# Kernel tuning notes

Hardware: AMD Instinct MI355X
Metric: run time of the kernel (lower is better)

Reference implementation:

```python
import jax, jax.numpy as jnp
import numpy as np

N = 20000      # nodes
E = 320000     # edges
S = 256        # scalar (0e) channels of irreps_feature
F = 960        # full irreps_feature dim (256x0e+128x1e+64x2e)
NB = 32        # number_of_basis
CUT = 5.0      # max_radius


def setup_inputs() -> dict:
    key = jax.random.key(0)
    ks = jax.random.split(key, 24)
    def w(k, shape):
        return jax.random.normal(k, shape, jnp.float32) / np.sqrt(shape[0])
    return {
        "node_feature": jax.random.normal(ks[0], (N, F), jnp.float32),
        "pos": jax.random.normal(ks[1], (N, 3), jnp.float32),
        "edge_index": jax.random.randint(ks[2], (2, E), 0, N),
        "W_ai1": w(ks[3], (S, S)), "b_ai1": jnp.zeros((S,), jnp.float32),
        "W_ai2": w(ks[4], (S, 1)), "b_ai2": jnp.zeros((1,), jnp.float32),
        "W_ci1": w(ks[5], (S, S)), "b_ci1": jnp.zeros((S,), jnp.float32),
        "W_ci2": w(ks[6], (S, 1)), "b_ci2": jnp.zeros((1,), jnp.float32),
        "W_sc": w(ks[7], (S, S)), "b_sc": jnp.zeros((S,), jnp.float32),
        "W_ed": w(ks[8], (NB, S)), "b_ed": jnp.zeros((S,), jnp.float32),
        "W_b1": w(ks[9], (3 * S, S)), "b_b1": jnp.zeros((S,), jnp.float32),
        "W_b2": w(ks[10], (S, 1)), "b_b2": jnp.zeros((1,), jnp.float32),
    }


def _rbf(d):
    # ExpNormalSmearing (torchmd-net), cutoff_lower=0, cutoff_upper=CUT, non-trainable
    start = np.exp(-CUT)
    means = jnp.linspace(start, 1.0, NB, dtype=jnp.float32)
    beta = jnp.float32(((2.0 / NB) * (1.0 - start)) ** -2)
    cosine_cut = 0.5 * (jnp.cos(np.pi * d / CUT) + 1.0) * (d < CUT)
    return cosine_cut[:, None] * jnp.exp(-beta * (jnp.exp(-d)[:, None] - means) ** 2)


def reference(node_feature, pos, edge_index,
              W_ai1, b_ai1, W_ai2, b_ai2,
              W_ci1, b_ci1, W_ci2, b_ci2,
              W_sc, b_sc, W_ed, b_ed,
              W_b1, b_b1, W_b2, b_b2):
    # LinearRS(irreps_feature -> 0e) only touches the 0e block (first S channels)
    scal = node_feature[:, :S]
    silu = jax.nn.silu

    log_ai = silu(scal @ W_ai1 + b_ai1) @ W_ai2 + b_ai2          # [N,1]
    ai = jnp.exp(log_ai)
    log_ci = silu(scal @ W_ci1 + b_ci1) @ W_ci2 + b_ci2          # [N,1]
    ci = jnp.exp(log_ci)

    src, dst = edge_index[0], edge_index[1]
    rel = pos[dst] - pos[src]                                     # [E,3]
    norm = jnp.linalg.norm(rel, axis=1, keepdims=True)            # [E,1]
    rhat = rel / (norm + 1e-8)
    emb = _rbf(norm[:, 0])                                        # [E,NB]

    node_sc = scal @ W_sc + b_sc                                  # project once, gather [N,S]
    src_f = node_sc[src]
    dst_f = node_sc[dst]
    edge_f = emb @ W_ed + b_ed
    edge_feature = jnp.concatenate([src_f, dst_f, edge_f], axis=-1)  # [E,3S]
    bij = silu(edge_feature @ W_b1 + b_b1) @ W_b2 + b_b2          # [E,1]

    # edge softmax over incoming edges of dst, with extra ci mass
    bmax = jax.ops.segment_max(bij, dst, num_segments=N)
    bmax = jnp.where(jnp.isneginf(bmax), 0.0, bmax)
    bij_exp = jnp.exp(bij - bmax[dst])
    bsum = jax.ops.segment_sum(bij_exp, dst, num_segments=N) + ci  # [N,1]
    gamma = bij_exp / (bsum[dst] + 1e-7)                           # [E,1]

    bij_prime = gamma * ai[dst]                                    # [E,1]
    outer = rhat[:, :, None] * rhat[:, None, :]                    # [E,3,3]
    contrib = jax.ops.segment_sum(bij_prime[:, :, None] * outer, dst, num_segments=N)  # [N,3,3]

    eye3 = jnp.eye(3, dtype=pos.dtype)
    sigma = ai[:, :, None] * eye3 - contrib + 1e-6 * eye3          # [N,3,3]
    sum_gamma = jax.ops.segment_sum(gamma, dst, num_segments=N)    # [N,1]
    return sigma, ai, sum_gamma
```

## Files before the change

### kernel.cpp

```cpp
#include <hip/hip_runtime.h>
#include <math.h>

#define N_NODES 20000
#define E_EDGES 320000
#define F_DIM   960
#define S_DIM   256
#define QTAB    2048
#define ASTRIDE 264
#define CAP     64
#define CPAD    66

typedef __attribute__((ext_vector_type(8))) short short8;
typedef __attribute__((ext_vector_type(4))) float f32x4;

__device__ __forceinline__ float siluf(float x) {
    return x / (1.0f + __expf(-x));
}

__device__ __forceinline__ unsigned short bf16rn(float x) {
    unsigned u = __float_as_uint(x);
    return (unsigned short)((u + 0x7FFFu + ((u >> 16) & 1u)) >> 16);
}

__device__ __forceinline__ void bf16x8_to_f32(short8 v8, float* o) {
    union { short8 s; uint4 u; } cv; cv.s = v8;
    o[0] = __uint_as_float(cv.u.x << 16);
    o[1] = __uint_as_float(cv.u.x & 0xffff0000u);
    o[2] = __uint_as_float(cv.u.y << 16);
    o[3] = __uint_as_float(cv.u.y & 0xffff0000u);
    o[4] = __uint_as_float(cv.u.z << 16);
    o[5] = __uint_as_float(cv.u.z & 0xffff0000u);
    o[6] = __uint_as_float(cv.u.w << 16);
    o[7] = __uint_as_float(cv.u.w & 0xffff0000u);
}

__global__ void prep_kernel(const float* __restrict__ W_sc, const float* __restrict__ W_ed,
                            const float* __restrict__ W_b1, const float* __restrict__ b_sc,
                            const float* __restrict__ b_ed, const float* __restrict__ b_b1,
                            const float* __restrict__ W_ai1, const float* __restrict__ W_ci1,
                            float* __restrict__ Bcat, float* __restrict__ We, float* __restrict__ c0,
                            int* __restrict__ cnt)
{
    int idx = blockIdx.x * 256 + threadIdx.x;
    if (idx < N_NODES) cnt[idx] = 0;
    if (idx < 256 * 1024) {
        int k = idx >> 10, j = idx & 1023;
        float s = 0.0f;
        if (j < 256) {
            for (int m = 0; m < 256; ++m) s += W_sc[k * 256 + m] * W_b1[m * 256 + j];
        } else if (j < 512) {
            int jj = j - 256;
            for (int m = 0; m < 256; ++m) s += W_sc[k * 256 + m] * W_b1[(256 + m) * 256 + jj];
        } else if (j < 768) {
            s = W_ai1[k * 256 + (j - 512)];
        } else {
            s = W_ci1[k * 256 + (j - 768)];
        }
        Bcat[idx] = s;
    } else if (idx < 256 * 1024 + 32 * 256) {
        int t = idx - 256 * 1024;
        int p = t >> 8, j = t & 255;
        float s = 0.0f;
        for (int m = 0; m < 256; ++m) s += W_ed[p * 256 + m] * W_b1[(512 + m) * 256 + j];
        We[t] = s;
    } else if (idx < 256 * 1024 + 32 * 256 + 256) {
        int j = idx - 256 * 1024 - 32 * 256;
        float s = b_b1[j];
        for (int m = 0; m < 256; ++m) {
            s += b_sc[m] * (W_b1[m * 256 + j] + W_b1[(256 + m) * 256 + j]);
            s += b_ed[m] * W_b1[(512 + m) * 256 + j];
        }
        c0[j] = s;
    }
}

__global__ void aux_kernel(const int* __restrict__ ei, int* __restrict__ cnt, int* __restrict__ rank,
                           const float* __restrict__ Bcat, unsigned short* __restrict__ Bpack,
                           const float* __restrict__ We, unsigned short* __restrict__ Tab,
                           const float* __restrict__ nf, unsigned short* __restrict__ scalp)
{
    int b = blockIdx.x;
    if (b < 1250) {
        int i = b * 256 + threadIdx.x;
        rank[i] = atomicAdd(&cnt[ei[E_EDGES + i]], 1);
    } else if (b < 1378) {
        int idx = (b - 1250) * 256 + threadIdx.x;
        int kq = idx & 3, j = (idx >> 2) & 1023, t = idx >> 12;
        #pragma unroll
        for (int jj = 0; jj < 8; ++jj)
            Bpack[idx * 8 + jj] = bf16rn(Bcat[(t * 32 + kq * 8 + jj) * 1024 + j]);
    } else if (b < 3426) {
        int idx = (b - 1378) * 256 + threadIdx.x;
        int q = idx >> 8, j = idx & 255;
        float nrm = 5.0f * (float)q / (float)(QTAB - 1);
        const float start = 0.006737946999085467f;
        const float mustep = (1.0f - start) / 31.0f;
        const float bx = (2.0f / 32.0f) * (1.0f - start);
        const float beta = 1.0f / (bx * bx);
        const float PI_F = 3.14159265358979323846f;
        float cc = (nrm < 5.0f) ? 0.5f * (cosf(PI_F * nrm * 0.2f) + 1.0f) : 0.0f;
        float t = expf(-nrm);
        float s = 0.0f;
        for (int k = 0; k < 32; ++k) {
            float dm = t - (start + (float)k * mustep);
            s += expf(-beta * dm * dm) * We[k * 256 + j];
        }
        Tab[idx] = bf16rn(cc * s);
    } else {
        int idx = (b - 3426) * 256 + threadIdx.x;
        int base = idx * 4;
        int n = base >> 8, k = base & 255;
        float4 a4 = *(const float4*)&nf[(size_t)n * F_DIM + k];
        ushort4 b4;
        b4.x = bf16rn(a4.x); b4.y = bf16rn(a4.y);
        b4.z = bf16rn(a4.z); b4.w = bf16rn(a4.w);
        *(ushort4*)&scalp[n * 256 + k] = b4;
    }
}

__global__ __launch_bounds__(1024) void scan_kernel(const int* __restrict__ cnt,
                                                    int* __restrict__ start)
{
    __shared__ int ps[1024];
    const int t = threadIdx.x;
    const int base = t * 20;
    int loc[20];
    int s = 0;
    #pragma unroll
    for (int i = 0; i < 20; ++i) {
        int n = (base + i < N_NODES) ? cnt[base + i] : 0;
        loc[i] = s; s += n;
    }
    ps[t] = s;
    __syncthreads();
    for (int off = 1; off < 1024; off <<= 1) {
        int v = (t >= off) ? ps[t - off] : 0;
        __syncthreads();
        ps[t] += v;
        __syncthreads();
    }
    int offset = ps[t] - s;
    #pragma unroll
    for (int i = 0; i < 20; ++i)
        if (base + i < N_NODES) start[base + i] = offset + loc[i];
}

__global__ void scatter_kernel(const int* __restrict__ ei, const int* __restrict__ start,
                               const int* __restrict__ rank, int* __restrict__ srcS)
{
    int i = blockIdx.x * 256 + threadIdx.x;
    if (i < E_EDGES) srcS[start[ei[E_EDGES + i]] + rank[i]] = ei[i];
}

__global__ __launch_bounds__(256) void node_mfma_kernel(
    const unsigned short* __restrict__ scalp, const unsigned short* __restrict__ Bpack,
    const float* __restrict__ c0,
    const float* __restrict__ b_ai1, const float* __restrict__ W_ai2, const float* __restrict__ b_ai2,
    const float* __restrict__ b_ci1, const float* __restrict__ W_ci2, const float* __restrict__ b_ci2,
    unsigned short* __restrict__ u, unsigned short* __restrict__ v,
    float* __restrict__ bsumseed, float* __restrict__ out_ai)
{
    __shared__ unsigned short A[32 * ASTRIDE];
    __shared__ float red[32 * 4];

    const int tid = threadIdx.x;
    const int w = tid >> 6, lane = tid & 63;
    const int bg = blockIdx.x & 3;
    const int m0 = (blockIdx.x >> 2) * 32;
    const int col16 = lane & 15, quad = lane >> 4;

    #pragma unroll
    for (int it = 0; it < 4; ++it) {
        int idx = (it * 256 + tid) * 8;
        int r = idx >> 8, c = idx & 255;
        *(uint4*)&A[r * ASTRIDE + c] = *(const uint4*)&scalp[(m0 + r) * 256 + c];
    }
    __syncthreads();

    f32x4 acc[2][4];
    #pragma unroll
    for (int mt = 0; mt < 2; ++mt)
        #pragma unroll
        for (int nt = 0; nt < 4; ++nt)
            acc[mt][nt] = (f32x4){0.0f, 0.0f, 0.0f, 0.0f};

    const int colbase = bg * 256 + w * 64;

    for (int t = 0; t < 8; ++t) {
        short8 af[2];
        #pragma unroll
        for (int mt = 0; mt < 2; ++mt)
            af[mt] = *(const short8*)&A[(mt * 16 + col16) * ASTRIDE + t * 32 + quad * 8];
        short8 bf[4];
        #pragma unroll
        for (int nt = 0; nt < 4; ++nt)
            bf[nt] = *(const short8*)&Bpack[(((t * 1024 + colbase + nt * 16 + col16) * 4) + quad) * 8];
        #pragma unroll
        for (int mt = 0; mt < 2; ++mt)
            #pragma unroll
            for (int nt = 0; nt < 4; ++nt)
                acc[mt][nt] = __builtin_amdgcn_mfma_f32_16x16x32_bf16(af[mt], bf[nt], acc[mt][nt], 0, 0, 0);
    }

    if (bg == 0) {
        #pragma unroll
        for (int nt = 0; nt < 4; ++nt) {
            int jl = w * 64 + nt * 16 + col16;
            float c0v = c0[jl];
            #pragma unroll
            for (int mt = 0; mt < 2; ++mt)
                #pragma unroll
                for (int reg = 0; reg < 4; ++reg)
                    u[(m0 + mt * 16 + quad * 4 + reg) * 256 + jl] = bf16rn(acc[mt][nt][reg] + c0v);
        }
    } else if (bg == 1) {
        #pragma unroll
        for (int nt = 0; nt < 4; ++nt) {
            int jl = w * 64 + nt * 16 + col16;
            #pragma unroll
            for (int mt = 0; mt < 2; ++mt)
                #pragma unroll
                for (int reg = 0; reg < 4; ++reg)
                    v[(m0 + mt * 16 + quad * 4 + reg) * 256 + jl] = bf16rn(acc[mt][nt][reg]);
        }
    } else {
        const float* b1 = (bg == 2) ? b_ai1 : b_ci1;
        const float* w2 = (bg == 2) ? W_ai2 : W_ci2;
        float s[2][4] = {{0, 0, 0, 0}, {0, 0, 0, 0}};
        #pragma unroll
        for (int nt = 0; nt < 4; ++nt) {
            int jl = w * 64 + nt * 16 + col16;
            float bb = b1[jl], ww = w2[jl];
            #pragma unroll
            for (int mt = 0; mt < 2; ++mt)
                #pragma unroll
                for (int reg = 0; reg < 4; ++reg)
                    s[mt][reg] += siluf(acc[mt][nt][reg] + bb) * ww;
        }
        #pragma unroll
        for (int off = 1; off < 16; off <<= 1) {
            #pragma unroll
            for (int mt = 0; mt < 2; ++mt)
                #pragma unroll
                for (int reg = 0; reg < 4; ++reg)
                    s[mt][reg] += __shfl_xor(s[mt][reg], off);
        }
        if (col16 == 0) {
            #pragma unroll
            for (int mt = 0; mt < 2; ++mt)
                #pragma unroll
                for (int reg = 0; reg < 4; ++reg)
                    red[(mt * 16 + quad * 4 + reg) * 4 + w] = s[mt][reg];
        }
        __syncthreads();
        if (tid < 32) {
            float sum = red[tid * 4] + red[tid * 4 + 1] + red[tid * 4 + 2] + red[tid * 4 + 3];
            if (bg == 2) out_ai[m0 + tid] = expf(sum + b_ai2[0]);
            else         bsumseed[m0 + tid] = expf(sum + b_ci2[0]) + 1e-7f;
        }
    }
}

__global__ __launch_bounds__(256) void edge_node_kernel(
    const int* __restrict__ start, const int* __restrict__ cnt, const int* __restrict__ srcS,
    const float* __restrict__ pos,
    const unsigned short* __restrict__ u, const unsigned short* __restrict__ v,
    const unsigned short* __restrict__ Tab, const float* __restrict__ W_b2, const float* __restrict__ b_b2,
    const float* __restrict__ bsumseed, const float* __restrict__ out_ai,
    float* __restrict__ out_sigma, float* __restrict__ out_sg)
{
    __shared__ float sb[16][CPAD];
    __shared__ float srx[16][CPAD];
    __shared__ float sry[16][CPAD];
    __shared__ float srz[16][CPAD];

    const int grp = threadIdx.x >> 4;
    const int l   = threadIdx.x & 15;
    const int g   = blockIdx.x * 16 + grp;
    const int st  = start[g];
    const int deg = min(cnt[g], CAP);

    float vch[16];
    bf16x8_to_f32(*(const short8*)&v[(size_t)g * 256 + l * 16], vch);
    bf16x8_to_f32(*(const short8*)&v[(size_t)g * 256 + l * 16 + 8], vch + 8);
    float w2c[16];
    #pragma unroll
    for (int c = 0; c < 16; c += 4)
        *(float4*)&w2c[c] = *(const float4*)&W_b2[l * 16 + c];
    const float bb2 = b_b2[0];
    const float gx = pos[3 * g + 0], gy = pos[3 * g + 1], gz = pos[3 * g + 2];
    const float xscale = (float)(QTAB - 1) * 0.2f;

    int s_cur = (deg > 0) ? srcS[st] : 0;
    float pxc = pos[3 * s_cur + 0], pyc = pos[3 * s_cur + 1], pzc = pos[3 * s_cur + 2];
    short8 u0c = *(const short8*)&u[(size_t)s_cur * 256 + l * 16];
    short8 u1c = *(const short8*)&u[(size_t)s_cur * 256 + l * 16 + 8];

    for (int i = 0; i < deg; ++i) {
        int s_nxt = (i + 1 < deg) ? srcS[st + i + 1] : s_cur;
        float pxn = pos[3 * s_nxt + 0], pyn = pos[3 * s_nxt + 1], pzn = pos[3 * s_nxt + 2];
        short8 u0n = *(const short8*)&u[(size_t)s_nxt * 256 + l * 16];
        short8 u1n = *(const short8*)&u[(size_t)s_nxt * 256 + l * 16 + 8];

        float px = gx - pxc, py = gy - pyc, pz = gz - pzc;
        float nrm = sqrtf(px * px + py * py + pz * pz);
        float inv = 1.0f / (nrm + 1e-8f);
        float rx = px * inv, ry = py * inv, rz = pz * inv;

        float x = nrm * xscale;
        int qi = (int)x;
        float f = x - (float)qi;
        if (qi >= QTAB - 1) { qi = QTAB - 2; f = 1.0f; }

        float acc = 0.0f;
        #pragma unroll
        for (int half = 0; half < 2; ++half) {
            float uf[8], t0f[8], t1f[8];
            bf16x8_to_f32(half ? u1c : u0c, uf);
            bf16x8_to_f32(*(const short8*)&Tab[(size_t)qi * 256 + l * 16 + half * 8], t0f);
            bf16x8_to_f32(*(const short8*)&Tab[(size_t)(qi + 1) * 256 + l * 16 + half * 8], t1f);
            #pragma unroll
            for (int c = 0; c < 8; ++c) {
                float h = uf[c] + vch[half * 8 + c] + t0f[c] + f * (t1f[c] - t0f[c]);
                float sig = __builtin_amdgcn_rcpf(1.0f + __expf(-h));
                acc += w2c[half * 8 + c] * h * sig;
            }
        }
        #pragma unroll
        for (int off = 1; off < 16; off <<= 1) acc += __shfl_xor(acc, off);

        if (l == 0) {
            sb[grp][i] = acc + bb2;
            srx[grp][i] = rx; sry[grp][i] = ry; srz[grp][i] = rz;
        }
        s_cur = s_nxt; pxc = pxn; pyc = pyn; pzc = pzn; u0c = u0n; u1c = u1n;
    }

    float m = -1e30f;
    for (int i = l; i < deg; i += 16) m = fmaxf(m, sb[grp][i]);
    #pragma unroll
    for (int off = 1; off < 16; off <<= 1) m = fmaxf(m, __shfl_xor(m, off));

    float ssum = 0.0f;
    for (int i = l; i < deg; i += 16) ssum += __expf(sb[grp][i] - m);
    #pragma unroll
    for (int off = 1; off < 16; off <<= 1) ssum += __shfl_xor(ssum, off);

    float invt = 1.0f / (ssum + bsumseed[g]);

    float a0 = 0, a1 = 0, a2 = 0, a3 = 0, a4 = 0, a5 = 0, a6 = 0;
    for (int i = l; i < deg; i += 16) {
        float gm = __expf(sb[grp][i] - m) * invt;
        float rx = srx[grp][i], ry = sry[grp][i], rz = srz[grp][i];
        a0 += gm * rx * rx; a1 += gm * ry * ry; a2 += gm * rz * rz;
        a3 += gm * rx * ry; a4 += gm * rx * rz; a5 += gm * ry * rz;
        a6 += gm;
    }
    #pragma unroll
    for (int off = 1; off < 16; off <<= 1) {
        a0 += __shfl_xor(a0, off); a1 += __shfl_xor(a1, off);
        a2 += __shfl_xor(a2, off); a3 += __shfl_xor(a3, off);
        a4 += __shfl_xor(a4, off); a5 += __shfl_xor(a5, off);
        a6 += __shfl_xor(a6, off);
    }

    if (l == 0) {
        float ai = out_ai[g];
        float* sg = &out_sigma[g * 9];
        float d0 = ai + 1e-6f;
        sg[0] = d0 - ai * a0;
        sg[1] = -ai * a3;
        sg[2] = -ai * a4;
        sg[3] = -ai * a3;
        sg[4] = d0 - ai * a1;
        sg[5] = -ai * a5;
        sg[6] = -ai * a4;
        sg[7] = -ai * a5;
        sg[8] = d0 - ai * a2;
        out_sg[g] = a6;
    }
}

extern "C" void kernel_launch(void* const* d_in, const int* in_sizes, int n_in,
                              void* d_out, int out_size, void* d_ws, size_t ws_size,
                              hipStream_t stream)
{
    const float* nf    = (const float*)d_in[0];
    const float* pos   = (const float*)d_in[1];
    const int*   ei    = (const int*)  d_in[2];
    const float* W_ai1 = (const float*)d_in[3];
    const float* b_ai1 = (const float*)d_in[4];
    const float* W_ai2 = (const float*)d_in[5];
    const float* b_ai2 = (const float*)d_in[6];
    const float* W_ci1 = (const float*)d_in[7];
    const float* b_ci1 = (const float*)d_in[8];
    const float* W_ci2 = (const float*)d_in[9];
    const float* b_ci2 = (const float*)d_in[10];
    const float* W_sc  = (const float*)d_in[11];
    const float* b_sc  = (const float*)d_in[12];
    const float* W_ed  = (const float*)d_in[13];
    const float* b_ed  = (const float*)d_in[14];
    const float* W_b1  = (const float*)d_in[15];
    const float* b_b1  = (const float*)d_in[16];
    const float* W_b2  = (const float*)d_in[17];
    const float* b_b2  = (const float*)d_in[18];

    char* pb = (char*)d_ws;
    auto alloc = [&](size_t bytes) -> void* {
        void* r = (void*)pb;
        pb += (bytes + 255) & ~(size_t)255;
        return r;
    };
    float*          Bcat    = (float*)         alloc(262144 * 4);
    float*          We      = (float*)         alloc(8192 * 4);
    float*          c0      = (float*)         alloc(256 * 4);
    unsigned short* Tab     = (unsigned short*)alloc((size_t)QTAB * 256 * 2);
    unsigned short* Bpack   = (unsigned short*)alloc((size_t)256 * 1024 * 2);
    unsigned short* scalp   = (unsigned short*)alloc((size_t)N_NODES * 256 * 2);
    unsigned short* u       = (unsigned short*)alloc((size_t)N_NODES * 256 * 2);
    unsigned short* v       = (unsigned short*)alloc((size_t)N_NODES * 256 * 2);
    float*          bsumseed= (float*)         alloc((size_t)N_NODES * 4);
    int*            cnt     = (int*)           alloc((size_t)N_NODES * 4);
    int*            startA  = (int*)           alloc((size_t)N_NODES * 4);
    int*            rank    = (int*)           alloc((size_t)E_EDGES * 4);
    int*            srcS    = (int*)           alloc((size_t)E_EDGES * 4);

    float* out       = (float*)d_out;
    float* out_sigma = out;
    float* out_ai    = out + N_NODES * 9;
    float* out_sg    = out + N_NODES * 10;

    prep_kernel<<<1058, 256, 0, stream>>>(W_sc, W_ed, W_b1, b_sc, b_ed, b_b1, W_ai1, W_ci1,
                                          Bcat, We, c0, cnt);
    aux_kernel<<<8426, 256, 0, stream>>>(ei, cnt, rank, Bcat, Bpack, We, Tab, nf, scalp);
    scan_kernel<<<1, 1024, 0, stream>>>(cnt, startA);
    scatter_kernel<<<1250, 256, 0, stream>>>(ei, startA, rank, srcS);
    node_mfma_kernel<<<2500, 256, 0, stream>>>(scalp, Bpack, c0, b_ai1, W_ai2, b_ai2,
                                               b_ci1, W_ci2, b_ci2, u, v, bsumseed, out_ai);
    edge_node_kernel<<<1250, 256, 0, stream>>>(startA, cnt, srcS, pos, u, v, Tab, W_b2, b_b2,
                                               bsumseed, out_ai, out_sigma, out_sg);
}
```

Before: 323.1 us.

## Fuse scatter and table-diff into node GEMM kernel, use fp32 u and RBF tables

Merges the edge scatter kernel and a new table-difference pass into the node MFMA launch as extra blocks, which removes one kernel launch. Each node block now computes all 1024 output columns, one wave per output group, instead of four blocks per row tile, so the cross-wave shared-memory reduction goes away. The u projection and RBF lookup table are now kept in fp32 with a precomputed delta table, which removes bf16 unpacking and one subtraction in the edge loop. In exchange, per-edge u gathers and table reads move twice as many bytes, and each wave holds many more accumulator registers.

```diff
diff --git a/kernel.cpp b/kernel.cpp
--- a/kernel.cpp
+++ b/kernel.cpp
@@ -76,7 +76,7 @@
 
 __global__ void aux_kernel(const int* __restrict__ ei, int* __restrict__ cnt, int* __restrict__ rank,
                            const float* __restrict__ Bcat, unsigned short* __restrict__ Bpack,
-                           const float* __restrict__ We, unsigned short* __restrict__ Tab,
+                           const float* __restrict__ We, float* __restrict__ TabV,
                            const float* __restrict__ nf, unsigned short* __restrict__ scalp)
 {
     int b = blockIdx.x;
@@ -105,7 +105,7 @@
             float dm = t - (start + (float)k * mustep);
             s += expf(-beta * dm * dm) * We[k * 256 + j];
         }
-        Tab[idx] = bf16rn(cc * s);
+        TabV[idx] = cc * s;
     } else {
         int idx = (b - 3426) * 256 + threadIdx.x;
         int base = idx * 4;
@@ -145,28 +145,33 @@
         if (base + i < N_NODES) start[base + i] = offset + loc[i];
 }
 
-__global__ void scatter_kernel(const int* __restrict__ ei, const int* __restrict__ start,
-                               const int* __restrict__ rank, int* __restrict__ srcS)
-{
-    int i = blockIdx.x * 256 + threadIdx.x;
-    if (i < E_EDGES) srcS[start[ei[E_EDGES + i]] + rank[i]] = ei[i];
-}
-
-__global__ __launch_bounds__(256) void node_mfma_kernel(
+__global__ __launch_bounds__(256) void mid_kernel(
     const unsigned short* __restrict__ scalp, const unsigned short* __restrict__ Bpack,
     const float* __restrict__ c0,
     const float* __restrict__ b_ai1, const float* __restrict__ W_ai2, const float* __restrict__ b_ai2,
     const float* __restrict__ b_ci1, const float* __restrict__ W_ci2, const float* __restrict__ b_ci2,
-    unsigned short* __restrict__ u, unsigned short* __restrict__ v,
-    float* __restrict__ bsumseed, float* __restrict__ out_ai)
+    float* __restrict__ u, unsigned short* __restrict__ v,
+    float* __restrict__ bsumseed, float* __restrict__ out_ai,
+    const int* __restrict__ ei, const int* __restrict__ start, const int* __restrict__ rank,
+    int* __restrict__ srcS,
+    const float* __restrict__ TabV, float* __restrict__ TabD)
 {
     __shared__ unsigned short A[32 * ASTRIDE];
-    __shared__ float red[32 * 4];
-
     const int tid = threadIdx.x;
+
+    if (blockIdx.x >= 625) {
+        if (blockIdx.x < 1875) {
+            int i = (blockIdx.x - 625) * 256 + tid;
+            srcS[start[ei[E_EDGES + i]] + rank[i]] = ei[i];
+        } else {
+            int idx = (blockIdx.x - 1875) * 256 + tid;
+            TabD[idx] = (idx < (QTAB - 1) * 256) ? TabV[idx + 256] - TabV[idx] : 0.0f;
+        }
+        return;
+    }
+
     const int w = tid >> 6, lane = tid & 63;
-    const int bg = blockIdx.x & 3;
-    const int m0 = (blockIdx.x >> 2) * 32;
+    const int m0 = blockIdx.x * 32;
     const int col16 = lane & 15, quad = lane >> 4;
 
     #pragma unroll
@@ -177,59 +182,56 @@
     }
     __syncthreads();
 
-    f32x4 acc[2][4];
+    f32x4 acc[2][16];
     #pragma unroll
     for (int mt = 0; mt < 2; ++mt)
         #pragma unroll
-        for (int nt = 0; nt < 4; ++nt)
+        for (int nt = 0; nt < 16; ++nt)
             acc[mt][nt] = (f32x4){0.0f, 0.0f, 0.0f, 0.0f};
 
-    const int colbase = bg * 256 + w * 64;
+    const int colbase = w * 256;
 
     for (int t = 0; t < 8; ++t) {
         short8 af[2];
         #pragma unroll
         for (int mt = 0; mt < 2; ++mt)
             af[mt] = *(const short8*)&A[(mt * 16 + col16) * ASTRIDE + t * 32 + quad * 8];
-        short8 bf[4];
-        #pragma unroll
-        for (int nt = 0; nt < 4; ++nt)
-            bf[nt] = *(const short8*)&Bpack[(((t * 1024 + colbase + nt * 16 + col16) * 4) + quad) * 8];
-        #pragma unroll
-        for (int mt = 0; mt < 2; ++mt)
-            #pragma unroll
-            for (int nt = 0; nt < 4; ++nt)
-                acc[mt][nt] = __builtin_amdgcn_mfma_f32_16x16x32_bf16(af[mt], bf[nt], acc[mt][nt], 0, 0, 0);
-    }
-
-    if (bg == 0) {
-        #pragma unroll
-        for (int nt = 0; nt < 4; ++nt) {
-            int jl = w * 64 + nt * 16 + col16;
+        #pragma unroll
+        for (int nt = 0; nt < 16; ++nt) {
+            short8 bf = *(const short8*)&Bpack[(((t * 1024 + colbase + nt * 16 + col16) * 4) + quad) * 8];
+            acc[0][nt] = __builtin_amdgcn_mfma_f32_16x16x32_bf16(af[0], bf, acc[0][nt], 0, 0, 0);
+            acc[1][nt] = __builtin_amdgcn_mfma_f32_16x16x32_bf16(af[1], bf, acc[1][nt], 0, 0, 0);
+        }
+    }
+
+    if (w == 0) {
+        #pragma unroll
+        for (int nt = 0; nt < 16; ++nt) {
+            int jl = nt * 16 + col16;
             float c0v = c0[jl];
             #pragma unroll
             for (int mt = 0; mt < 2; ++mt)
                 #pragma unroll
                 for (int reg = 0; reg < 4; ++reg)
-                    u[(m0 + mt * 16 + quad * 4 + reg) * 256 + jl] = bf16rn(acc[mt][nt][reg] + c0v);
-        }
-    } else if (bg == 1) {
-        #pragma unroll
-        for (int nt = 0; nt < 4; ++nt) {
-            int jl = w * 64 + nt * 16 + col16;
+                    u[(size_t)(m0 + mt * 16 + quad * 4 + reg) * 256 + jl] = acc[mt][nt][reg] + c0v;
+        }
+    } else if (w == 1) {
+        #pragma unroll
+        for (int nt = 0; nt < 16; ++nt) {
+            int jl = nt * 16 + col16;
             #pragma unroll
             for (int mt = 0; mt < 2; ++mt)
                 #pragma unroll
                 for (int reg = 0; reg < 4; ++reg)
-                    v[(m0 + mt * 16 + quad * 4 + reg) * 256 + jl] = bf16rn(acc[mt][nt][reg]);
+                    v[(size_t)(m0 + mt * 16 + quad * 4 + reg) * 256 + jl] = bf16rn(acc[mt][nt][reg]);
         }
     } else {
-        const float* b1 = (bg == 2) ? b_ai1 : b_ci1;
-        const float* w2 = (bg == 2) ? W_ai2 : W_ci2;
+        const float* b1 = (w == 2) ? b_ai1 : b_ci1;
+        const float* w2 = (w == 2) ? W_ai2 : W_ci2;
         float s[2][4] = {{0, 0, 0, 0}, {0, 0, 0, 0}};
         #pragma unroll
-        for (int nt = 0; nt < 4; ++nt) {
-            int jl = w * 64 + nt * 16 + col16;
+        for (int nt = 0; nt < 16; ++nt) {
+            int jl = nt * 16 + col16;
             float bb = b1[jl], ww = w2[jl];
             #pragma unroll
             for (int mt = 0; mt < 2; ++mt)
@@ -249,14 +251,11 @@
             #pragma unroll
             for (int mt = 0; mt < 2; ++mt)
                 #pragma unroll
-                for (int reg = 0; reg < 4; ++reg)
-                    red[(mt * 16 + quad * 4 + reg) * 4 + w] = s[mt][reg];
-        }
-        __syncthreads();
-        if (tid < 32) {
-            float sum = red[tid * 4] + red[tid * 4 + 1] + red[tid * 4 + 2] + red[tid * 4 + 3];
-            if (bg == 2) out_ai[m0 + tid] = expf(sum + b_ai2[0]);
-            else         bsumseed[m0 + tid] = expf(sum + b_ci2[0]) + 1e-7f;
+                for (int reg = 0; reg < 4; ++reg) {
+                    int row = m0 + mt * 16 + quad * 4 + reg;
+                    if (w == 2) out_ai[row] = expf(s[mt][reg] + b_ai2[0]);
+                    else        bsumseed[row] = expf(s[mt][reg] + b_ci2[0]) + 1e-7f;
+                }
         }
     }
 }
@@ -264,8 +263,9 @@
 __global__ __launch_bounds__(256) void edge_node_kernel(
     const int* __restrict__ start, const int* __restrict__ cnt, const int* __restrict__ srcS,
     const float* __restrict__ pos,
-    const unsigned short* __restrict__ u, const unsigned short* __restrict__ v,
-    const unsigned short* __restrict__ Tab, const float* __restrict__ W_b2, const float* __restrict__ b_b2,
+    const float* __restrict__ u, const unsigned short* __restrict__ v,
+    const float* __restrict__ TabV, const float* __restrict__ TabD,
+    const float* __restrict__ W_b2, const float* __restrict__ b_b2,
     const float* __restrict__ bsumseed, const float* __restrict__ out_ai,
     float* __restrict__ out_sigma, float* __restrict__ out_sg)
 {
@@ -293,14 +293,18 @@
 
     int s_cur = (deg > 0) ? srcS[st] : 0;
     float pxc = pos[3 * s_cur + 0], pyc = pos[3 * s_cur + 1], pzc = pos[3 * s_cur + 2];
-    short8 u0c = *(const short8*)&u[(size_t)s_cur * 256 + l * 16];
-    short8 u1c = *(const short8*)&u[(size_t)s_cur * 256 + l * 16 + 8];
+    float4 uc[4];
+    #pragma unroll
+    for (int cq = 0; cq < 4; ++cq)
+        uc[cq] = *(const float4*)&u[(size_t)s_cur * 256 + l * 16 + cq * 4];
 
     for (int i = 0; i < deg; ++i) {
         int s_nxt = (i + 1 < deg) ? srcS[st + i + 1] : s_cur;
         float pxn = pos[3 * s_nxt + 0], pyn = pos[3 * s_nxt + 1], pzn = pos[3 * s_nxt + 2];
-        short8 u0n = *(const short8*)&u[(size_t)s_nxt * 256 + l * 16];
-        short8 u1n = *(const short8*)&u[(size_t)s_nxt * 256 + l * 16 + 8];
+        float4 un[4];
+        #pragma unroll
+        for (int cq = 0; cq < 4; ++cq)
+            un[cq] = *(const float4*)&u[(size_t)s_nxt * 256 + l * 16 + cq * 4];
 
         float px = gx - pxc, py = gy - pyc, pz = gz - pzc;
         float nrm = sqrtf(px * px + py * py + pz * pz);
@@ -314,17 +318,18 @@
 
         float acc = 0.0f;
         #pragma unroll
-        for (int half = 0; half < 2; ++half) {
-            float uf[8], t0f[8], t1f[8];
-            bf16x8_to_f32(half ? u1c : u0c, uf);
-            bf16x8_to_f32(*(const short8*)&Tab[(size_t)qi * 256 + l * 16 + half * 8], t0f);
-            bf16x8_to_f32(*(const short8*)&Tab[(size_t)(qi + 1) * 256 + l * 16 + half * 8], t1f);
-            #pragma unroll
-            for (int c = 0; c < 8; ++c) {
-                float h = uf[c] + vch[half * 8 + c] + t0f[c] + f * (t1f[c] - t0f[c]);
-                float sig = __builtin_amdgcn_rcpf(1.0f + __expf(-h));
-                acc += w2c[half * 8 + c] * h * sig;
-            }
+        for (int cq = 0; cq < 4; ++cq) {
+            float4 tv = *(const float4*)&TabV[(size_t)qi * 256 + l * 16 + cq * 4];
+            float4 td = *(const float4*)&TabD[(size_t)qi * 256 + l * 16 + cq * 4];
+            float4 uu = uc[cq];
+            float h0 = uu.x + vch[cq * 4 + 0] + tv.x + f * td.x;
+            float h1 = uu.y + vch[cq * 4 + 1] + tv.y + f * td.y;
+            float h2 = uu.z + vch[cq * 4 + 2] + tv.z + f * td.z;
+            float h3 = uu.w + vch[cq * 4 + 3] + tv.w + f * td.w;
+            acc += w2c[cq * 4 + 0] * h0 * __builtin_amdgcn_rcpf(1.0f + __expf(-h0));
+            acc += w2c[cq * 4 + 1] * h1 * __builtin_amdgcn_rcpf(1.0f + __expf(-h1));
+            acc += w2c[cq * 4 + 2] * h2 * __builtin_amdgcn_rcpf(1.0f + __expf(-h2));
+            acc += w2c[cq * 4 + 3] * h3 * __builtin_amdgcn_rcpf(1.0f + __expf(-h3));
         }
         #pragma unroll
         for (int off = 1; off < 16; off <<= 1) acc += __shfl_xor(acc, off);
@@ -333,7 +338,8 @@
             sb[grp][i] = acc + bb2;
             srx[grp][i] = rx; sry[grp][i] = ry; srz[grp][i] = rz;
         }
-        s_cur = s_nxt; pxc = pxn; pyc = pyn; pzc = pzn; u0c = u0n; u1c = u1n;
+        s_cur = s_nxt; pxc = pxn; pyc = pyn; pzc = pzn;
+        uc[0] = un[0]; uc[1] = un[1]; uc[2] = un[2]; uc[3] = un[3];
     }
 
     float m = -1e30f;
@@ -414,10 +420,11 @@
     float*          Bcat    = (float*)         alloc(262144 * 4);
     float*          We      = (float*)         alloc(8192 * 4);
     float*          c0      = (float*)         alloc(256 * 4);
-    unsigned short* Tab     = (unsigned short*)alloc((size_t)QTAB * 256 * 2);
+    float*          TabV    = (float*)         alloc((size_t)QTAB * 256 * 4);
+    float*          TabD    = (float*)         alloc((size_t)QTAB * 256 * 4);
     unsigned short* Bpack   = (unsigned short*)alloc((size_t)256 * 1024 * 2);
     unsigned short* scalp   = (unsigned short*)alloc((size_t)N_NODES * 256 * 2);
-    unsigned short* u       = (unsigned short*)alloc((size_t)N_NODES * 256 * 2);
+    float*          u       = (float*)         alloc((size_t)N_NODES * 256 * 4);
     unsigned short* v       = (unsigned short*)alloc((size_t)N_NODES * 256 * 2);
     float*          bsumseed= (float*)         alloc((size_t)N_NODES * 4);
     int*            cnt     = (int*)           alloc((size_t)N_NODES * 4);
@@ -432,11 +439,11 @@
 
     prep_kernel<<<1058, 256, 0, stream>>>(W_sc, W_ed, W_b1, b_sc, b_ed, b_b1, W_ai1, W_ci1,
                                           Bcat, We, c0, cnt);
-    aux_kernel<<<8426, 256, 0, stream>>>(ei, cnt, rank, Bcat, Bpack, We, Tab, nf, scalp);
+    aux_kernel<<<8426, 256, 0, stream>>>(ei, cnt, rank, Bcat, Bpack, We, TabV, nf, scalp);
     scan_kernel<<<1, 1024, 0, stream>>>(cnt, startA);
-    scatter_kernel<<<1250, 256, 0, stream>>>(ei, startA, rank, srcS);
-    node_mfma_kernel<<<2500, 256, 0, stream>>>(scalp, Bpack, c0, b_ai1, W_ai2, b_ai2,
-                                               b_ci1, W_ci2, b_ci2, u, v, bsumseed, out_ai);
-    edge_node_kernel<<<1250, 256, 0, stream>>>(startA, cnt, srcS, pos, u, v, Tab, W_b2, b_b2,
-                                               bsumseed, out_ai, out_sigma, out_sg);
-}
+    mid_kernel<<<3923, 256, 0, stream>>>(scalp, Bpack, c0, b_ai1, W_ai2, b_ai2,
+                                         b_ci1, W_ci2, b_ci2, u, v, bsumseed, out_ai,
+                                         ei, startA, rank, srcS, TabV, TabD);
+    edge_node_kernel<<<1250, 256, 0, stream>>>(startA, cnt, srcS, pos, u, v, TabV, TabD,
+                                               W_b2, b_b2, bsumseed, out_ai, out_sigma, out_sg);
+}
```

After: 379.3 us. 1.17x slower.
